# Kernel optimization log

Hardware: AMD Instinct MI355X
Metric: run time of the kernel (lower is better)

The kernel has to match this reference:

```python
import jax, jax.numpy as jnp
import numpy as np

DK = 128  # key/query head dim (also value dim)

def setup_inputs() -> dict:
    key = jax.random.key(0)
    k1, k2, k3, k4 = jax.random.split(key, 4)
    query = jax.random.normal(k1, (8, 512, 28, 28), dtype=jnp.float32)
    support = jax.random.normal(k2, (16, 512, 28, 28), dtype=jnp.float32)
    Wk = jax.random.normal(k3, (128, 512), dtype=jnp.float32) * (1.0 / np.sqrt(512.0))
    Wv = jax.random.normal(k4, (128, 512), dtype=jnp.float32) * (1.0 / np.sqrt(512.0))
    return {"query": query, "support": support, "Wk": Wk, "Wv": Wv}

def reference(query, support, Wk, Wv):
    B, D, H, W = query.shape
    N, Ds, Hs, Ws = support.shape
    q_flat = query.reshape(B, D, H * W)        # b d u
    s_flat = support.reshape(N, Ds, Hs * Ws)   # n d v
    # 1x1 convs == channel projections (query_head is aliased to key_head)
    q = jnp.einsum('kd,bdu->bku', Wk, q_flat)            # B dk u
    query_value = jnp.einsum('kd,bdu->bku', Wv, q_flat)  # B dv u
    support_key = jnp.einsum('kd,ndv->nkv', Wk, s_flat)  # N dk v
    support_value = jnp.einsum('kd,ndv->nkv', Wv, s_flat)  # N dv v
    scores = jnp.einsum('bku,nkv->bnuv', q, support_key) / jnp.sqrt(jnp.float32(DK))
    # first softmax over dim=3 in the source is dead code (overwritten); effective
    # attention is softmax over the support-class axis n (dim=1)
    attn = jax.nn.softmax(scores, axis=1)  # B N u v
    # note: u is summed out here, exactly as in the source einsum
    query_aligned = jnp.einsum('bnuv,nkv->bkv', attn, support_value)  # B dv v
    a = query_aligned.transpose(0, 2, 1)   # B v dv
    b = query_value.transpose(0, 2, 1)     # B u dv
    # cdist(p=2)**2 == squared euclidean distances; compute without forming diffs
    a2 = jnp.sum(a * a, axis=-1)  # B v
    b2 = jnp.sum(b * b, axis=-1)  # B u
    ab = jnp.einsum('bpd,brd->bpr', a, b)  # B v u
    d2 = jnp.maximum(a2[:, :, None] + b2[:, None, :] - 2.0 * ab, 0.0)
    P, R = d2.shape[1], d2.shape[2]
    return jnp.sum(d2, axis=(1, 2)) / (P * R)  # (B,)
```

## Files before the change

kernel.cpp:

```cpp
#include <hip/hip_runtime.h>

#define U_CNT 784
#define DKH   128
#define DD    512
#define NS    16

typedef short bf16x8 __attribute__((ext_vector_type(8)));
typedef float f32x4  __attribute__((ext_vector_type(4)));

__device__ __forceinline__ unsigned short f2bf(float f) {
  unsigned u = __builtin_bit_cast(unsigned, f);
  u += 0x7fffu + ((u >> 16) & 1u);
  return (unsigned short)(u >> 16);
}


__global__ void cast_w(const float* __restrict__ Wk, const float* __restrict__ Wv,
                       unsigned short* __restrict__ Wkv) {
  int base = (blockIdx.x * 256 + threadIdx.x) * 8;
#pragma unroll
  for (int i = 0; i < 8; ++i) {
    int e = base + i;
    int ko = e >> 9, d = e & 511;
    float v = (ko < 128) ? Wk[ko * 512 + d] : Wv[(ko - 128) * 512 + d];
    Wkv[e] = f2bf(v);
  }
}

__global__ __launch_bounds__(256)
void proj_kernel(const float* __restrict__ query, const float* __restrict__ support,
                 const unsigned short* __restrict__ Wkv,
                 unsigned short* __restrict__ q_f, unsigned short* __restrict__ sk_f,
                 float* __restrict__ sv_t, float* __restrict__ S1p, float* __restrict__ S2p) {
  int pt = blockIdx.x;
  int m  = blockIdx.y;
  int wave = threadIdx.x >> 6;
  int l = threadIdx.x & 63;
  int col = l & 15, rowg = l >> 4;
  int p = pt * 16 + col;
  const float* X = (m < 8) ? (query + (size_t)m * DD * U_CNT)
                           : (support + (size_t)(m - 8) * DD * U_CNT);
  f32x4 acc[4];
  f32x4 zero = {0.f, 0.f, 0.f, 0.f};
#pragma unroll
  for (int rr = 0; rr < 4; ++rr) acc[rr] = zero;

  for (int ds = 0; ds < 16; ++ds) {
    int d0 = ds * 32 + rowg * 8;
    bf16x8 bfrag;
#pragma unroll
    for (int j = 0; j < 8; ++j) {
      float x = X[(size_t)(d0 + j) * U_CNT + p];
      bfrag[j] = (short)f2bf(x);
    }
#pragma unroll
    for (int rr = 0; rr < 4; ++rr) {
      int r = wave * 4 + rr;
      const bf16x8* ap = (const bf16x8*)(Wkv + (size_t)(r * 16 + col) * DD + d0);
      acc[rr] = __builtin_amdgcn_mfma_f32_16x16x32_bf16(*ap, bfrag, acc[rr], 0, 0, 0);
    }
  }

  if (m < 8) {
    if (wave < 2) {
#pragma unroll
      for (int rr = 0; rr < 4; ++rr) {
        int r = wave * 4 + rr;
        const float sc = 0.08838834764831845f;
        ushort4 o;
        o.x = f2bf(acc[rr][0] * sc); o.y = f2bf(acc[rr][1] * sc);
        o.z = f2bf(acc[rr][2] * sc); o.w = f2bf(acc[rr][3] * sc);
        size_t off = (size_t)m * 100352 + (size_t)pt * 2048 +
                     (size_t)(2 * r + (rowg >> 1)) * 128 + col * 8 + (rowg & 1) * 4;
        *(ushort4*)(q_f + off) = o;
      }
    } else {
      float s1 = 0.f;
#pragma unroll
      for (int rr = 0; rr < 4; ++rr) {
        int r = wave * 4 + rr;
#pragma unroll
        for (int j = 0; j < 4; ++j) {
          float x = acc[rr][j];
          s1 += x * x;
          x += __shfl_xor(x, 1, 64); x += __shfl_xor(x, 2, 64);
          x += __shfl_xor(x, 4, 64); x += __shfl_xor(x, 8, 64);
          if (col == 0)
            S2p[((size_t)pt * 8 + m) * DKH + (r - 8) * 16 + rowg * 4 + j] = x;
        }
      }
#pragma unroll
      for (int o = 32; o >= 1; o >>= 1) s1 += __shfl_xor(s1, o, 64);
      if (l == 0) S1p[((wave - 2) * 49 + pt) * 8 + m] = s1;
    }
  } else {
    int img = m - 8;
    if (wave < 2) {
#pragma unroll
      for (int rr = 0; rr < 4; ++rr) {
        int r = wave * 4 + rr;
        ushort4 o;
        o.x = f2bf(acc[rr][0]); o.y = f2bf(acc[rr][1]);
        o.z = f2bf(acc[rr][2]); o.w = f2bf(acc[rr][3]);
        size_t off = (size_t)p * 2048 +
                     (size_t)(2 * r + (rowg >> 1)) * 128 + img * 8 + (rowg & 1) * 4;
        *(ushort4*)(sk_f + off) = o;
      }
    } else {
#pragma unroll
      for (int rr = 0; rr < 4; ++rr) {
        int r = wave * 4 + rr;
        int kb = (r - 8) * 16 + rowg * 4;
        float4 o = make_float4(acc[rr][0], acc[rr][1], acc[rr][2], acc[rr][3]);
        *(float4*)(sv_t + (size_t)(img * U_CNT + p) * DKH + kb) = o;
      }
    }
  }
}

__global__ __launch_bounds__(256, 4)
void score_kernel(const unsigned short* __restrict__ q_f,
                  const unsigned short* __restrict__ sk_f,
                  float* __restrict__ w_part) {
  int bx = blockIdx.x;
  int vb = bx % 49;
  int uc = (bx / 49) & 3;
  int b  = bx / 196;
  int wv = threadIdx.x >> 6;
  int l  = threadIdx.x & 63;
  int col = l & 15, rowg = l >> 4;
  int vbase = vb * 16 + wv * 4;

  bf16x8 A[4][4];
#pragma unroll
  for (int v = 0; v < 4; ++v) {
    const unsigned short* ap = sk_f + (size_t)(vbase + v) * 2048 + rowg * 128 + col * 8;
#pragma unroll
    for (int s = 0; s < 4; ++s) A[v][s] = *(const bf16x8*)(ap + s * 512);
  }

  float wl[4][4];
#pragma unroll
  for (int v = 0; v < 4; ++v)
#pragma unroll
    for (int j = 0; j < 4; ++j) wl[v][j] = 0.f;

  int ut0 = (uc == 0) ? 0 : uc * 12 + 1;
  int cnt = (uc == 0) ? 13 : 12;
  const unsigned short* qb = q_f + (size_t)b * 100352 + rowg * 128 + col * 8;
  f32x4 zero = {0.f, 0.f, 0.f, 0.f};

  const unsigned short* qp0 = qb + (size_t)ut0 * 2048;
  bf16x8 B0 = *(const bf16x8*)(qp0);
  bf16x8 B1 = *(const bf16x8*)(qp0 + 512);
  bf16x8 B2 = *(const bf16x8*)(qp0 + 1024);
  bf16x8 B3 = *(const bf16x8*)(qp0 + 1536);

  for (int it = 0; it < cnt; ++it) {
    int nit = (it + 1 < cnt) ? it + 1 : it;
    const unsigned short* qp = qb + (size_t)(ut0 + nit) * 2048;
    bf16x8 N0 = *(const bf16x8*)(qp);
    bf16x8 N1 = *(const bf16x8*)(qp + 512);
    bf16x8 N2 = *(const bf16x8*)(qp + 1024);
    bf16x8 N3 = *(const bf16x8*)(qp + 1536);

    f32x4 acc[4];
#pragma unroll
    for (int v = 0; v < 4; ++v) acc[v] = zero;
#pragma unroll
    for (int v = 0; v < 4; ++v)
      acc[v] = __builtin_amdgcn_mfma_f32_16x16x32_bf16(A[v][0], B0, acc[v], 0, 0, 0);
#pragma unroll
    for (int v = 0; v < 4; ++v)
      acc[v] = __builtin_amdgcn_mfma_f32_16x16x32_bf16(A[v][1], B1, acc[v], 0, 0, 0);
#pragma unroll
    for (int v = 0; v < 4; ++v)
      acc[v] = __builtin_amdgcn_mfma_f32_16x16x32_bf16(A[v][2], B2, acc[v], 0, 0, 0);
#pragma unroll
    for (int v = 0; v < 4; ++v)
      acc[v] = __builtin_amdgcn_mfma_f32_16x16x32_bf16(A[v][3], B3, acc[v], 0, 0, 0);
#pragma unroll
    for (int v = 0; v < 4; ++v) {
      float e0 = __expf(acc[v][0]), e1 = __expf(acc[v][1]);
      float e2 = __expf(acc[v][2]), e3 = __expf(acc[v][3]);
      float ps = (e0 + e1) + (e2 + e3);
      ps += __shfl_xor(ps, 16, 64);
      ps += __shfl_xor(ps, 32, 64);
      float r = __builtin_amdgcn_rcpf(ps);
      wl[v][0] += e0 * r; wl[v][1] += e1 * r;
      wl[v][2] += e2 * r; wl[v][3] += e3 * r;
    }
    B0 = N0; B1 = N1; B2 = N2; B3 = N3;
  }
#pragma unroll
  for (int v = 0; v < 4; ++v)
#pragma unroll
    for (int j = 0; j < 4; ++j) {
      float x = wl[v][j];
      x += __shfl_xor(x, 1, 64); x += __shfl_xor(x, 2, 64);
      x += __shfl_xor(x, 4, 64); x += __shfl_xor(x, 8, 64);
      wl[v][j] = x;
    }
  __shared__ float wst[4][4][16];
#pragma unroll
  for (int v = 0; v < 4; ++v)
    if (col == v) {
#pragma unroll
      for (int j = 0; j < 4; ++j) wst[wv][v][rowg * 4 + j] = wl[v][j];
    }
  __syncthreads();
  int t = threadIdx.x;
  int vl = t >> 4, c = t & 15;
  w_part[(((size_t)uc * 8 + b) * U_CNT + vb * 16 + vl) * NS + c] =
      wst[vl >> 2][vl & 3][c];
}

__global__ __launch_bounds__(256)
void align_kernel(const float* __restrict__ w_part, const float* __restrict__ sv_t,
                  float* __restrict__ T1p, float* __restrict__ T2p) {
  int vt2 = blockIdx.x;
  int t = threadIdx.x;
  __shared__ float w_sh[2][8][16];
  {
    int vl = t >> 7, b = (t >> 4) & 7, n = t & 15;
    float s = 0.f;
#pragma unroll
    for (int uc = 0; uc < 4; ++uc)
      s += w_part[(((size_t)uc * 8 + b) * U_CNT + vt2 * 2 + vl) * NS + n];
    w_sh[vl][b][n] = s;
  }
  __syncthreads();
  int k = t & 127, vl = t >> 7;
  int v = vt2 * 2 + vl;
  float a[8];
#pragma unroll
  for (int b = 0; b < 8; ++b) a[b] = 0.f;
#pragma unroll
  for (int n = 0; n < NS; ++n) {
    float s = sv_t[((size_t)n * U_CNT + v) * DKH + k];
#pragma unroll
    for (int b = 0; b < 8; ++b) a[b] += w_sh[vl][b][n] * s;
  }
  __shared__ float red[8][128];
  if (vl == 1) {
#pragma unroll
    for (int b = 0; b < 8; ++b) red[b][k] = a[b];
  }
  __syncthreads();
  if (vl == 0) {
#pragma unroll
    for (int b = 0; b < 8; ++b)
      T2p[((size_t)vt2 * 8 + b) * DKH + k] = a[b] + red[b][k];
  }
  __shared__ float sw1[4][8];
#pragma unroll
  for (int b = 0; b < 8; ++b) {
    float x = a[b] * a[b];
#pragma unroll
    for (int o = 32; o >= 1; o >>= 1) x += __shfl_xor(x, o, 64);
    if ((t & 63) == 0) sw1[t >> 6][b] = x;
  }
  __syncthreads();
  if (t < 8) T1p[vt2 * 8 + t] = sw1[0][t] + sw1[1][t] + sw1[2][t] + sw1[3][t];
}

__global__ __launch_bounds__(256)
void reduce_partials(const float* __restrict__ S1p, const float* __restrict__ T1p,
                     const float* __restrict__ S2p, const float* __restrict__ T2p,
                     float* __restrict__ S2, float* __restrict__ T2,
                     float* __restrict__ ST1) {
  __shared__ float smem[264];
  int bx = blockIdx.x, t = threadIdx.x;
  if (bx < 32) {
    int b = bx >> 2, kq = bx & 3;
    int kl = t & 31, g = t >> 5;
    int k = kq * 32 + kl;
    float s = 0.f;
    for (int w = g; w < 392; w += 8)
      s += T2p[((size_t)w * 8 + b) * DKH + k];
    smem[g * 32 + kl] = s;
    __syncthreads();
    if (t < 32) {
      float v = 0.f;
#pragma unroll
      for (int g2 = 0; g2 < 8; ++g2) v += smem[g2 * 32 + t];
      T2[b * DKH + kq * 32 + t] = v;
    }
  } else {
    int b = bx - 32;
    int k = t & 127, h = t >> 7;
    float s = 0.f;
    for (int w = h; w < 49; w += 2)
      s += S2p[((size_t)w * 8 + b) * DKH + k];
    if (h == 1) smem[k] = s;
    __syncthreads();
    if (h == 0) S2[b * DKH + k] = s + smem[k];
    float c = 0.f;
    for (int i = t; i < 98; i += 256)  c += S1p[i * 8 + b];
    for (int i = t; i < 392; i += 256) c += T1p[i * 8 + b];
#pragma unroll
    for (int o = 32; o >= 1; o >>= 1) c += __shfl_xor(c, o, 64);
    if ((t & 63) == 0) smem[256 + (t >> 6)] = c;
    __syncthreads();
    if (t == 0) ST1[b] = smem[256] + smem[257] + smem[258] + smem[259];
  }
}

__global__ void final_kernel(const float* __restrict__ S2, const float* __restrict__ T2,
                             const float* __restrict__ ST1, float* __restrict__ out) {
  int b = blockIdx.x, t = threadIdx.x;
  float p = S2[b * DKH + t] * T2[b * DKH + t];
#pragma unroll
  for (int o = 32; o >= 1; o >>= 1) p += __shfl_xor(p, o, 64);
  __shared__ float s2[2];
  if ((t & 63) == 0) s2[t >> 6] = p;
  __syncthreads();
  if (t == 0)
    out[b] = (784.0f * ST1[b] - 2.0f * (s2[0] + s2[1])) * (1.0f / (784.0f * 784.0f));
}

extern "C" void kernel_launch(void* const* d_in, const int* in_sizes, int n_in,
                              void* d_out, int out_size, void* d_ws, size_t ws_size,
                              hipStream_t stream) {
  const float* query   = (const float*)d_in[0];
  const float* support = (const float*)d_in[1];
  const float* Wk      = (const float*)d_in[2];
  const float* Wv      = (const float*)d_in[3];
  float* out = (float*)d_out;
  char* ws = (char*)d_ws;

  unsigned short* Wkv  = (unsigned short*)(ws + 0);
  unsigned short* q_f  = (unsigned short*)(ws + 262144);
  unsigned short* sk_f = (unsigned short*)(ws + 1867776);
  float*          sv_t = (float*)(ws + 5079040);
  float*          w_part = (float*)(ws + 11501568);
  float*          S1p  = (float*)(ws + 14712832);
  float*          T1p  = (float*)(ws + 14716928);
  float*          S2p  = (float*)(ws + 14733312);
  float*          T2p  = (float*)(ws + 14934016);
  float*          S2   = (float*)(ws + 16539648);
  float*          T2   = (float*)(ws + 16543744);
  float*          ST1  = (float*)(ws + 16547840);
  if (ws_size < (size_t)16548000) return;

  cast_w<<<64, 256, 0, stream>>>(Wk, Wv, Wkv);
  proj_kernel<<<dim3(49, 24), 256, 0, stream>>>(query, support, Wkv, q_f, sk_f, sv_t, S1p, S2p);
  score_kernel<<<1568, 256, 0, stream>>>(q_f, sk_f, w_part);
  align_kernel<<<392, 256, 0, stream>>>(w_part, sv_t, T1p, T2p);
  reduce_partials<<<40, 256, 0, stream>>>(S1p, T1p, S2p, T2p, S2, T2, ST1);
  final_kernel<<<8, 128, 0, stream>>>(S2, T2, ST1, out);
}
```

Measured before the change: 175.8 us.

## Stage projection input tile in LDS with float4 loads and prefetch weights

The projection kernel now loads its whole 512x16 input tile into shared memory up front with coalesced float4 global loads. It transposes the tile so each lane reads its 8 consecutive channels as two float4 LDS reads, replacing 8 strided scalar global loads per step. Weight fragments for the next k-step are prefetched into registers (double buffering), and launch bounds now request 4 blocks per SM. The cost is about 33KB of LDS per block, which may limit occupancy, plus a barrier and more register pressure.

```diff
diff --git a/kernel.cpp b/kernel.cpp
--- a/kernel.cpp
+++ b/kernel.cpp
@@ -27,38 +27,71 @@
   }
 }
 
-__global__ __launch_bounds__(256)
+__global__ __launch_bounds__(256, 4)
 void proj_kernel(const float* __restrict__ query, const float* __restrict__ support,
                  const unsigned short* __restrict__ Wkv,
                  unsigned short* __restrict__ q_f, unsigned short* __restrict__ sk_f,
                  float* __restrict__ sv_t, float* __restrict__ S1p, float* __restrict__ S2p) {
+  constexpr int ROWW = 516;
+  __shared__ float xs[16 * ROWW];
   int pt = blockIdx.x;
   int m  = blockIdx.y;
-  int wave = threadIdx.x >> 6;
-  int l = threadIdx.x & 63;
-  int col = l & 15, rowg = l >> 4;
-  int p = pt * 16 + col;
+  int tid = threadIdx.x;
   const float* X = (m < 8) ? (query + (size_t)m * DD * U_CNT)
                            : (support + (size_t)(m - 8) * DD * U_CNT);
+  int p0 = pt * 16;
+
+  {
+    int pi = tid & 3;
+    int dbase = tid >> 2;
+#pragma unroll
+    for (int pass = 0; pass < 8; ++pass) {
+      int d = pass * 64 + dbase;
+      float4 v = *(const float4*)(X + (size_t)d * U_CNT + p0 + pi * 4);
+      xs[(pi * 4 + 0) * ROWW + d] = v.x;
+      xs[(pi * 4 + 1) * ROWW + d] = v.y;
+      xs[(pi * 4 + 2) * ROWW + d] = v.z;
+      xs[(pi * 4 + 3) * ROWW + d] = v.w;
+    }
+  }
+  __syncthreads();
+
+  int wave = tid >> 6;
+  int l = tid & 63;
+  int col = l & 15, rowg = l >> 4;
+  int p = p0 + col;
+
   f32x4 acc[4];
   f32x4 zero = {0.f, 0.f, 0.f, 0.f};
 #pragma unroll
   for (int rr = 0; rr < 4; ++rr) acc[rr] = zero;
 
+  bf16x8 Acur[4], Anxt[4];
+#pragma unroll
+  for (int rr = 0; rr < 4; ++rr)
+    Acur[rr] = *(const bf16x8*)(Wkv + (size_t)((wave * 4 + rr) * 16 + col) * DD + rowg * 8);
+
   for (int ds = 0; ds < 16; ++ds) {
+    int nd0 = ((ds + 1) & 15) * 32 + rowg * 8;
+#pragma unroll
+    for (int rr = 0; rr < 4; ++rr)
+      Anxt[rr] = *(const bf16x8*)(Wkv + (size_t)((wave * 4 + rr) * 16 + col) * DD + nd0);
+
     int d0 = ds * 32 + rowg * 8;
+    const float* xp = &xs[col * ROWW + d0];
+    float4 xa = *(const float4*)(xp);
+    float4 xb = *(const float4*)(xp + 4);
     bf16x8 bfrag;
-#pragma unroll
-    for (int j = 0; j < 8; ++j) {
-      float x = X[(size_t)(d0 + j) * U_CNT + p];
-      bfrag[j] = (short)f2bf(x);
-    }
-#pragma unroll
-    for (int rr = 0; rr < 4; ++rr) {
-      int r = wave * 4 + rr;
-      const bf16x8* ap = (const bf16x8*)(Wkv + (size_t)(r * 16 + col) * DD + d0);
-      acc[rr] = __builtin_amdgcn_mfma_f32_16x16x32_bf16(*ap, bfrag, acc[rr], 0, 0, 0);
-    }
+    bfrag[0] = (short)f2bf(xa.x); bfrag[1] = (short)f2bf(xa.y);
+    bfrag[2] = (short)f2bf(xa.z); bfrag[3] = (short)f2bf(xa.w);
+    bfrag[4] = (short)f2bf(xb.x); bfrag[5] = (short)f2bf(xb.y);
+    bfrag[6] = (short)f2bf(xb.z); bfrag[7] = (short)f2bf(xb.w);
+
+#pragma unroll
+    for (int rr = 0; rr < 4; ++rr)
+      acc[rr] = __builtin_amdgcn_mfma_f32_16x16x32_bf16(Acur[rr], bfrag, acc[rr], 0, 0, 0);
+#pragma unroll
+    for (int rr = 0; rr < 4; ++rr) Acur[rr] = Anxt[rr];
   }
 
   if (m < 8) {
```

Result: no change. 175.2 us (-0.3%).

## Tile projection kernel over 112 positions with double-buffered LDS staging

Applied to the files above, without the earlier changes.

The projection kernel now handles 112 spatial positions per block instead of 16. It stages the fp32 input through a double-buffered shared-memory tile using coalesced float4 loads, and reuses each weight fragment across 7 position subtiles. This is meant to remove the strided scalar global reads and the repeated weight reads of the old per-16-column blocks. In exchange the grid shrinks from 1176 to 168 blocks with launch bounds of one block per SM and heavy register/LDS use. That leaves many of the GPU's CUs idle and risks lower occupancy. Partial-sum counts in reduce_partials are adjusted to match.

```diff
diff --git a/kernel.cpp b/kernel.cpp
--- a/kernel.cpp
+++ b/kernel.cpp
@@ -27,37 +27,81 @@
   }
 }
 
-__global__ __launch_bounds__(256)
+__global__ __launch_bounds__(256, 1)
 void proj_kernel(const float* __restrict__ query, const float* __restrict__ support,
                  const unsigned short* __restrict__ Wkv,
                  unsigned short* __restrict__ q_f, unsigned short* __restrict__ sk_f,
                  float* __restrict__ sv_t, float* __restrict__ S1p, float* __restrict__ S2p) {
-  int pt = blockIdx.x;
+  constexpr int PB = 112;
+  constexpr int DR = 128;
+  constexpr int ROWW = DR + 4;
+  __shared__ float xs[2][PB * ROWW];
+  int pc = blockIdx.x;
   int m  = blockIdx.y;
-  int wave = threadIdx.x >> 6;
-  int l = threadIdx.x & 63;
-  int col = l & 15, rowg = l >> 4;
-  int p = pt * 16 + col;
+  int tid = threadIdx.x;
+  int p0 = pc * PB;
   const float* X = (m < 8) ? (query + (size_t)m * DD * U_CNT)
                            : (support + (size_t)(m - 8) * DD * U_CNT);
-  f32x4 acc[4];
+  int drow = tid >> 1, pg = tid & 1;
+  const float* xrow = X + p0 + pg * 56;
+
+  float4 vbuf[14];
+  auto loadR = [&](int rd) {
+    const float* s = xrow + (size_t)(rd * DR + drow) * U_CNT;
+#pragma unroll
+    for (int i = 0; i < 14; ++i) vbuf[i] = *(const float4*)(s + i * 4);
+  };
+  auto storeR = [&](int bb) {
+    float* d0 = &xs[bb][(pg * 56) * ROWW + drow];
+#pragma unroll
+    for (int i = 0; i < 14; ++i) {
+      float* dp = d0 + (i * 4) * ROWW;
+      dp[0] = vbuf[i].x; dp[ROWW] = vbuf[i].y;
+      dp[2 * ROWW] = vbuf[i].z; dp[3 * ROWW] = vbuf[i].w;
+    }
+  };
+
+  int wave = tid >> 6, l = tid & 63;
+  int col = l & 15, rowg = l >> 4;
+
+  f32x4 acc[7][4];
   f32x4 zero = {0.f, 0.f, 0.f, 0.f};
 #pragma unroll
-  for (int rr = 0; rr < 4; ++rr) acc[rr] = zero;
-
-  for (int ds = 0; ds < 16; ++ds) {
-    int d0 = ds * 32 + rowg * 8;
-    bf16x8 bfrag;
-#pragma unroll
-    for (int j = 0; j < 8; ++j) {
-      float x = X[(size_t)(d0 + j) * U_CNT + p];
-      bfrag[j] = (short)f2bf(x);
-    }
-#pragma unroll
-    for (int rr = 0; rr < 4; ++rr) {
-      int r = wave * 4 + rr;
-      const bf16x8* ap = (const bf16x8*)(Wkv + (size_t)(r * 16 + col) * DD + d0);
-      acc[rr] = __builtin_amdgcn_mfma_f32_16x16x32_bf16(*ap, bfrag, acc[rr], 0, 0, 0);
+  for (int v7 = 0; v7 < 7; ++v7)
+#pragma unroll
+    for (int rr = 0; rr < 4; ++rr) acc[v7][rr] = zero;
+
+  loadR(0); storeR(0);
+  __syncthreads();
+  for (int rd = 0; rd < 4; ++rd) {
+    if (rd < 3) loadR(rd + 1);
+    int bb = rd & 1;
+#pragma unroll
+    for (int ds = 0; ds < 4; ++ds) {
+      int dl = ds * 32 + rowg * 8;
+      bf16x8 Af[4];
+#pragma unroll
+      for (int rr = 0; rr < 4; ++rr)
+        Af[rr] = *(const bf16x8*)(Wkv + (size_t)((wave * 4 + rr) * 16 + col) * DD + rd * DR + dl);
+#pragma unroll
+      for (int v7 = 0; v7 < 7; ++v7) {
+        const float* xp = &xs[bb][(v7 * 16 + col) * ROWW + dl];
+        float4 xa = *(const float4*)(xp);
+        float4 xb = *(const float4*)(xp + 4);
+        bf16x8 bf;
+        bf[0] = (short)f2bf(xa.x); bf[1] = (short)f2bf(xa.y);
+        bf[2] = (short)f2bf(xa.z); bf[3] = (short)f2bf(xa.w);
+        bf[4] = (short)f2bf(xb.x); bf[5] = (short)f2bf(xb.y);
+        bf[6] = (short)f2bf(xb.z); bf[7] = (short)f2bf(xb.w);
+#pragma unroll
+        for (int rr = 0; rr < 4; ++rr)
+          acc[v7][rr] = __builtin_amdgcn_mfma_f32_16x16x32_bf16(Af[rr], bf, acc[v7][rr], 0, 0, 0);
+      }
+    }
+    if (rd < 3) {
+      __syncthreads();
+      storeR((rd + 1) & 1);
+      __syncthreads();
     }
   }
 
@@ -67,12 +111,15 @@
       for (int rr = 0; rr < 4; ++rr) {
         int r = wave * 4 + rr;
         const float sc = 0.08838834764831845f;
-        ushort4 o;
-        o.x = f2bf(acc[rr][0] * sc); o.y = f2bf(acc[rr][1] * sc);
-        o.z = f2bf(acc[rr][2] * sc); o.w = f2bf(acc[rr][3] * sc);
-        size_t off = (size_t)m * 100352 + (size_t)pt * 2048 +
-                     (size_t)(2 * r + (rowg >> 1)) * 128 + col * 8 + (rowg & 1) * 4;
-        *(ushort4*)(q_f + off) = o;
+#pragma unroll
+        for (int v7 = 0; v7 < 7; ++v7) {
+          ushort4 o;
+          o.x = f2bf(acc[v7][rr][0] * sc); o.y = f2bf(acc[v7][rr][1] * sc);
+          o.z = f2bf(acc[v7][rr][2] * sc); o.w = f2bf(acc[v7][rr][3] * sc);
+          size_t off = (size_t)m * 100352 + (size_t)(pc * 7 + v7) * 2048 +
+                       (size_t)(2 * r + (rowg >> 1)) * 128 + col * 8 + (rowg & 1) * 4;
+          *(ushort4*)(q_f + off) = o;
+        }
       }
     } else {
       float s1 = 0.f;
@@ -81,17 +128,21 @@
         int r = wave * 4 + rr;
 #pragma unroll
         for (int j = 0; j < 4; ++j) {
-          float x = acc[rr][j];
-          s1 += x * x;
-          x += __shfl_xor(x, 1, 64); x += __shfl_xor(x, 2, 64);
-          x += __shfl_xor(x, 4, 64); x += __shfl_xor(x, 8, 64);
+          float xsum = 0.f;
+#pragma unroll
+          for (int v7 = 0; v7 < 7; ++v7) {
+            float x = acc[v7][rr][j];
+            s1 += x * x; xsum += x;
+          }
+          xsum += __shfl_xor(xsum, 1, 64); xsum += __shfl_xor(xsum, 2, 64);
+          xsum += __shfl_xor(xsum, 4, 64); xsum += __shfl_xor(xsum, 8, 64);
           if (col == 0)
-            S2p[((size_t)pt * 8 + m) * DKH + (r - 8) * 16 + rowg * 4 + j] = x;
+            S2p[((size_t)pc * 8 + m) * DKH + (r - 8) * 16 + rowg * 4 + j] = xsum;
         }
       }
 #pragma unroll
       for (int o = 32; o >= 1; o >>= 1) s1 += __shfl_xor(s1, o, 64);
-      if (l == 0) S1p[((wave - 2) * 49 + pt) * 8 + m] = s1;
+      if (l == 0) S1p[((wave - 2) * 7 + pc) * 8 + m] = s1;
     }
   } else {
     int img = m - 8;
@@ -99,20 +150,27 @@
 #pragma unroll
       for (int rr = 0; rr < 4; ++rr) {
         int r = wave * 4 + rr;
-        ushort4 o;
-        o.x = f2bf(acc[rr][0]); o.y = f2bf(acc[rr][1]);
-        o.z = f2bf(acc[rr][2]); o.w = f2bf(acc[rr][3]);
-        size_t off = (size_t)p * 2048 +
-                     (size_t)(2 * r + (rowg >> 1)) * 128 + img * 8 + (rowg & 1) * 4;
-        *(ushort4*)(sk_f + off) = o;
+#pragma unroll
+        for (int v7 = 0; v7 < 7; ++v7) {
+          ushort4 o;
+          o.x = f2bf(acc[v7][rr][0]); o.y = f2bf(acc[v7][rr][1]);
+          o.z = f2bf(acc[v7][rr][2]); o.w = f2bf(acc[v7][rr][3]);
+          size_t off = (size_t)(p0 + v7 * 16 + col) * 2048 +
+                       (size_t)(2 * r + (rowg >> 1)) * 128 + img * 8 + (rowg & 1) * 4;
+          *(ushort4*)(sk_f + off) = o;
+        }
       }
     } else {
 #pragma unroll
       for (int rr = 0; rr < 4; ++rr) {
         int r = wave * 4 + rr;
         int kb = (r - 8) * 16 + rowg * 4;
-        float4 o = make_float4(acc[rr][0], acc[rr][1], acc[rr][2], acc[rr][3]);
-        *(float4*)(sv_t + (size_t)(img * U_CNT + p) * DKH + kb) = o;
+#pragma unroll
+        for (int v7 = 0; v7 < 7; ++v7) {
+          int p = p0 + v7 * 16 + col;
+          float4 o = make_float4(acc[v7][rr][0], acc[v7][rr][1], acc[v7][rr][2], acc[v7][rr][3]);
+          *(float4*)(sv_t + (size_t)(img * U_CNT + p) * DKH + kb) = o;
+        }
       }
     }
   }
@@ -290,13 +348,13 @@
     int b = bx - 32;
     int k = t & 127, h = t >> 7;
     float s = 0.f;
-    for (int w = h; w < 49; w += 2)
+    for (int w = h; w < 7; w += 2)
       s += S2p[((size_t)w * 8 + b) * DKH + k];
     if (h == 1) smem[k] = s;
     __syncthreads();
     if (h == 0) S2[b * DKH + k] = s + smem[k];
     float c = 0.f;
-    for (int i = t; i < 98; i += 256)  c += S1p[i * 8 + b];
+    for (int i = t; i < 14; i += 256)  c += S1p[i * 8 + b];
     for (int i = t; i < 392; i += 256) c += T1p[i * 8 + b];
 #pragma unroll
     for (int o = 32; o >= 1; o >>= 1) c += __shfl_xor(c, o, 64);
@@ -344,7 +402,7 @@
   if (ws_size < (size_t)16548000) return;
 
   cast_w<<<64, 256, 0, stream>>>(Wk, Wv, Wkv);
-  proj_kernel<<<dim3(49, 24), 256, 0, stream>>>(query, support, Wkv, q_f, sk_f, sv_t, S1p, S2p);
+  proj_kernel<<<dim3(7, 24), 256, 0, stream>>>(query, support, Wkv, q_f, sk_f, sv_t, S1p, S2p);
   score_kernel<<<1568, 256, 0, stream>>>(q_f, sk_f, w_part);
   align_kernel<<<392, 256, 0, stream>>>(w_part, sv_t, T1p, T2p);
   reduce_partials<<<40, 256, 0, stream>>>(S1p, T1p, S2p, T2p, S2, T2, ST1);
```

New measurement: 162.0 us. -7.8%, faster.

## Pre-transpose inputs to bf16 fragment layout and use exp2 softmax

Applied to the files above, without the earlier changes.

Adds a transpose kernel that reads the fp32 query/support tensors with coalesced float4 loads, converts them to bf16 and writes them in MFMA-fragment order through swizzled LDS. The projection kernel then loads one contiguous bf16x8 per step with a one-step prefetch, replacing eight strided scalar loads and conversions. The query scale folds in log2(e) so the score kernel can call the hardware exp2 instead of __expf. The cost is an extra kernel launch and a round trip through a roughly 19 MB bf16 intermediate buffer, which doubles the workspace.

```diff
diff --git a/kernel.cpp b/kernel.cpp
--- a/kernel.cpp
+++ b/kernel.cpp
@@ -28,37 +28,73 @@
 }
 
 __global__ __launch_bounds__(256)
-void proj_kernel(const float* __restrict__ query, const float* __restrict__ support,
+void xpose_kernel(const float* __restrict__ query, const float* __restrict__ support,
+                  unsigned short* __restrict__ x_f) {
+  __shared__ unsigned short lds[784 * 34];
+  int s = blockIdx.x;
+  int m = blockIdx.y;
+  const float* X = (m < 8) ? (query + (size_t)m * DD * U_CNT)
+                           : (support + (size_t)(m - 8) * DD * U_CNT);
+  int tid = threadIdx.x;
+  for (int i = 0; i < 25; ++i) {
+    int idx = i * 256 + tid;
+    if (idx < 6272) {
+      int row = idx / 196, c4 = idx - row * 196;
+      float4 v = *(const float4*)(X + (size_t)(s * 32 + row) * U_CNT + c4 * 4);
+      float vv[4] = {v.x, v.y, v.z, v.w};
+#pragma unroll
+      for (int cc = 0; cc < 4; ++cc) {
+        int p = c4 * 4 + cc;
+        int sw = row ^ ((p & 15) << 1);
+        lds[p * 34 + sw] = f2bf(vv[cc]);
+      }
+    }
+  }
+  __syncthreads();
+  unsigned short* xb = x_f + (size_t)m * 401408;
+  for (int i = 0; i < 49; ++i) {
+    int idx = i * 256 + tid;
+    int pt = idx >> 8, rem = idx & 255;
+    int cl = rem >> 6, q2 = rem & 63, ul = q2 >> 2, jj = (q2 & 3) * 2;
+    int p = pt * 16 + ul;
+    int dl = cl * 8 + jj;
+    int sw = dl ^ ((p & 15) << 1);
+    ushort2 o = *(const ushort2*)(&lds[p * 34 + sw]);
+    *(ushort2*)(xb + (size_t)pt * 8192 + (s * 4 + cl) * 128 + ul * 8 + jj) = o;
+  }
+}
+
+__global__ __launch_bounds__(256, 4)
+void proj_kernel(const unsigned short* __restrict__ x_f,
                  const unsigned short* __restrict__ Wkv,
                  unsigned short* __restrict__ q_f, unsigned short* __restrict__ sk_f,
                  float* __restrict__ sv_t, float* __restrict__ S1p, float* __restrict__ S2p) {
   int pt = blockIdx.x;
   int m  = blockIdx.y;
-  int wave = threadIdx.x >> 6;
-  int l = threadIdx.x & 63;
+  int tid = threadIdx.x;
+  int wave = tid >> 6, l = tid & 63;
   int col = l & 15, rowg = l >> 4;
-  int p = pt * 16 + col;
-  const float* X = (m < 8) ? (query + (size_t)m * DD * U_CNT)
-                           : (support + (size_t)(m - 8) * DD * U_CNT);
+
+  const unsigned short* xb =
+      x_f + (size_t)m * 401408 + (size_t)pt * 8192 + rowg * 128 + col * 8;
   f32x4 acc[4];
   f32x4 zero = {0.f, 0.f, 0.f, 0.f};
 #pragma unroll
   for (int rr = 0; rr < 4; ++rr) acc[rr] = zero;
 
+  bf16x8 Bcur = *(const bf16x8*)(xb);
   for (int ds = 0; ds < 16; ++ds) {
-    int d0 = ds * 32 + rowg * 8;
-    bf16x8 bfrag;
-#pragma unroll
-    for (int j = 0; j < 8; ++j) {
-      float x = X[(size_t)(d0 + j) * U_CNT + p];
-      bfrag[j] = (short)f2bf(x);
-    }
-#pragma unroll
-    for (int rr = 0; rr < 4; ++rr) {
-      int r = wave * 4 + rr;
-      const bf16x8* ap = (const bf16x8*)(Wkv + (size_t)(r * 16 + col) * DD + d0);
-      acc[rr] = __builtin_amdgcn_mfma_f32_16x16x32_bf16(*ap, bfrag, acc[rr], 0, 0, 0);
-    }
+    int nds = (ds + 1 < 16) ? ds + 1 : ds;
+    bf16x8 Bnxt = *(const bf16x8*)(xb + nds * 512);
+    bf16x8 Af[4];
+#pragma unroll
+    for (int rr = 0; rr < 4; ++rr)
+      Af[rr] = *(const bf16x8*)(Wkv + (size_t)((wave * 4 + rr) * 16 + col) * DD +
+                                ds * 32 + rowg * 8);
+#pragma unroll
+    for (int rr = 0; rr < 4; ++rr)
+      acc[rr] = __builtin_amdgcn_mfma_f32_16x16x32_bf16(Af[rr], Bcur, acc[rr], 0, 0, 0);
+    Bcur = Bnxt;
   }
 
   if (m < 8) {
@@ -66,7 +102,7 @@
 #pragma unroll
       for (int rr = 0; rr < 4; ++rr) {
         int r = wave * 4 + rr;
-        const float sc = 0.08838834764831845f;
+        const float sc = 0.12751744f;
         ushort4 o;
         o.x = f2bf(acc[rr][0] * sc); o.y = f2bf(acc[rr][1] * sc);
         o.z = f2bf(acc[rr][2] * sc); o.w = f2bf(acc[rr][3] * sc);
@@ -102,7 +138,7 @@
         ushort4 o;
         o.x = f2bf(acc[rr][0]); o.y = f2bf(acc[rr][1]);
         o.z = f2bf(acc[rr][2]); o.w = f2bf(acc[rr][3]);
-        size_t off = (size_t)p * 2048 +
+        size_t off = (size_t)(pt * 16 + col) * 2048 +
                      (size_t)(2 * r + (rowg >> 1)) * 128 + img * 8 + (rowg & 1) * 4;
         *(ushort4*)(sk_f + off) = o;
       }
@@ -112,7 +148,7 @@
         int r = wave * 4 + rr;
         int kb = (r - 8) * 16 + rowg * 4;
         float4 o = make_float4(acc[rr][0], acc[rr][1], acc[rr][2], acc[rr][3]);
-        *(float4*)(sv_t + (size_t)(img * U_CNT + p) * DKH + kb) = o;
+        *(float4*)(sv_t + (size_t)(img * U_CNT + pt * 16 + col) * DKH + kb) = o;
       }
     }
   }
@@ -181,8 +217,10 @@
       acc[v] = __builtin_amdgcn_mfma_f32_16x16x32_bf16(A[v][3], B3, acc[v], 0, 0, 0);
 #pragma unroll
     for (int v = 0; v < 4; ++v) {
-      float e0 = __expf(acc[v][0]), e1 = __expf(acc[v][1]);
-      float e2 = __expf(acc[v][2]), e3 = __expf(acc[v][3]);
+      float e0 = __builtin_amdgcn_exp2f(acc[v][0]);
+      float e1 = __builtin_amdgcn_exp2f(acc[v][1]);
+      float e2 = __builtin_amdgcn_exp2f(acc[v][2]);
+      float e3 = __builtin_amdgcn_exp2f(acc[v][3]);
       float ps = (e0 + e1) + (e2 + e3);
       ps += __shfl_xor(ps, 16, 64);
       ps += __shfl_xor(ps, 32, 64);
@@ -334,17 +372,19 @@
   unsigned short* sk_f = (unsigned short*)(ws + 1867776);
   float*          sv_t = (float*)(ws + 5079040);
   float*          w_part = (float*)(ws + 11501568);
-  float*          S1p  = (float*)(ws + 14712832);
-  float*          T1p  = (float*)(ws + 14716928);
-  float*          S2p  = (float*)(ws + 14733312);
-  float*          T2p  = (float*)(ws + 14934016);
-  float*          S2   = (float*)(ws + 16539648);
-  float*          T2   = (float*)(ws + 16543744);
-  float*          ST1  = (float*)(ws + 16547840);
-  if (ws_size < (size_t)16548000) return;
+  unsigned short* x_f  = (unsigned short*)(ws + 13107200);
+  float*          S1p  = (float*)(ws + 32374784);
+  float*          T1p  = (float*)(ws + 32378880);
+  float*          S2p  = (float*)(ws + 32395264);
+  float*          T2p  = (float*)(ws + 32595968);
+  float*          S2   = (float*)(ws + 34201600);
+  float*          T2   = (float*)(ws + 34205696);
+  float*          ST1  = (float*)(ws + 34209792);
+  if (ws_size < (size_t)34210000) return;
 
   cast_w<<<64, 256, 0, stream>>>(Wk, Wv, Wkv);
-  proj_kernel<<<dim3(49, 24), 256, 0, stream>>>(query, support, Wkv, q_f, sk_f, sv_t, S1p, S2p);
+  xpose_kernel<<<dim3(16, 24), 256, 0, stream>>>(query, support, x_f);
+  proj_kernel<<<dim3(49, 24), 256, 0, stream>>>(x_f, Wkv, q_f, sk_f, sv_t, S1p, S2p);
   score_kernel<<<1568, 256, 0, stream>>>(q_f, sk_f, w_part);
   align_kernel<<<392, 256, 0, stream>>>(w_part, sv_t, T1p, T2p);
   reduce_partials<<<40, 256, 0, stream>>>(S1p, T1p, S2p, T2p, S2, T2, ST1);
```

New measurement: 187.3 us. +6.5%, slower.
